# Optimization experiments

Measured on AMD Instinct MI355X. Metric: run time of the kernel, lower is better.

## Reference

```python
import jax, jax.numpy as jnp
import numpy as np

B, SQ, SK, HID, H, D = 2, 2048, 2048, 1024, 16, 64
LN_EPS = 1e-12


def _sinusoid(seq_len):
    # [1,1,S,D]: first half sin, second half cos (RoFormer convention)
    pos = np.arange(seq_len, dtype=np.float32)[:, None]
    inv_freq = 1.0 / (10000.0 ** (np.arange(0, D, 2, dtype=np.float32) / D))
    ang = pos * inv_freq  # [S, D/2]
    return jnp.asarray(np.concatenate([np.sin(ang), np.cos(ang)], axis=-1)[None, None], dtype=jnp.float32)


def setup_inputs() -> dict:
    key = jax.random.key(0)
    ks = jax.random.split(key, 12)
    w = lambda k, shape: jax.random.normal(k, shape, dtype=jnp.float32) * 0.02
    return {
        "hidden_states": jax.random.normal(ks[0], (B, SQ, HID), dtype=jnp.float32),
        "encoder_hidden_states": jax.random.normal(ks[1], (B, SK, HID), dtype=jnp.float32),
        "encoder_attention_mask": jnp.zeros((B, 1, 1, SK), dtype=jnp.float32),  # additive mask
        "sinusoidal_pos": _sinusoid(SQ),
        "c_sinusoidal_pos": _sinusoid(SK),
        "Wq": w(ks[2], (HID, HID)), "bq": jnp.zeros((HID,), jnp.float32),
        "Wk": w(ks[3], (HID, HID)), "bk": jnp.zeros((HID,), jnp.float32),
        "Wv": w(ks[4], (HID, HID)), "bv": jnp.zeros((HID,), jnp.float32),
        "Wd": w(ks[5], (HID, HID)), "bd": jnp.zeros((HID,), jnp.float32),
        "ln_gamma": jnp.ones((HID,), jnp.float32),
        "ln_beta": jnp.zeros((HID,), jnp.float32),
    }


def apply_rope(sinusoidal_pos, layer):
    # sinusoidal_pos: [1,1,S,D] = sin||cos halves; layer: [B,H,S,D]
    sin, cos = jnp.split(sinusoidal_pos, 2, axis=-1)
    sin_pos = jnp.stack([sin, sin], axis=-1).reshape(sinusoidal_pos.shape)
    cos_pos = jnp.stack([cos, cos], axis=-1).reshape(sinusoidal_pos.shape)
    rot = jnp.stack([-layer[..., 1::2], layer[..., ::2]], axis=-1).reshape(layer.shape)
    return layer * cos_pos + rot * sin_pos


def _heads(x):
    b, s, _ = x.shape
    return x.reshape(b, s, H, D).transpose(0, 2, 1, 3)  # [B,H,S,D]


def reference(hidden_states, encoder_hidden_states, encoder_attention_mask,
              sinusoidal_pos, c_sinusoidal_pos,
              Wq, bq, Wk, bk, Wv, bv, Wd, bd, ln_gamma, ln_beta):
    q = _heads(hidden_states @ Wq.T + bq)
    k = _heads(encoder_hidden_states @ Wk.T + bk)
    v = _heads(encoder_hidden_states @ Wv.T + bv)
    q = apply_rope(sinusoidal_pos, q)
    k = apply_rope(c_sinusoidal_pos, k)

    scores = jnp.einsum("bhqd,bhkd->bhqk", q, k) / jnp.sqrt(jnp.float32(D))
    scores = scores + encoder_attention_mask  # broadcast [B,1,1,SK]
    probs = jax.nn.softmax(scores, axis=-1)
    ctx = jnp.einsum("bhqk,bhkd->bhqd", probs, v)
    ctx = ctx.transpose(0, 2, 1, 3).reshape(hidden_states.shape[0], -1, HID)

    proj = ctx @ Wd.T + bd
    x = hidden_states + proj
    mu = jnp.mean(x, axis=-1, keepdims=True)
    var = jnp.mean(jnp.square(x - mu), axis=-1, keepdims=True)
    return (x - mu) / jnp.sqrt(var + LN_EPS) * ln_gamma + ln_beta
```

## Files before the change

### kernel.cpp

```cpp
#include <hip/hip_runtime.h>

typedef __attribute__((ext_vector_type(8))) short short8;
typedef __attribute__((ext_vector_type(4))) float f32x4;
typedef __attribute__((ext_vector_type(16))) float f32x16;

#define LOG2E 1.4426950408889634f
#define QSCALE 0.18033688011112042f

#define ASM_VMCNT2() asm volatile("s_waitcnt vmcnt(2)" ::: "memory")
#define ASM_VMCNT1() asm volatile("s_waitcnt vmcnt(1)" ::: "memory")
#define ASM_VMCNT0() asm volatile("s_waitcnt vmcnt(0)" ::: "memory")
#define ASM_LGKM0()  asm volatile("s_waitcnt lgkmcnt(0)" ::: "memory")

static __device__ __forceinline__ unsigned short f2bf(float f){
  unsigned u = __builtin_bit_cast(unsigned, f);
  u += 0x7FFFu + ((u>>16)&1u);
  return (unsigned short)(u>>16);
}
static __device__ __forceinline__ float bf2f(unsigned short u){
  return __builtin_bit_cast(float, ((unsigned)u)<<16);
}

static __device__ __forceinline__ void async16(const void* g, const void* l){
  __builtin_amdgcn_global_load_lds(
      (const __attribute__((address_space(1))) unsigned*)(unsigned long long)g,
      (__attribute__((address_space(3))) unsigned*)(unsigned)(unsigned long long)l,
      16, 0, 0);
}

__global__ __launch_bounds__(256) void prep_kernel(
    const float* __restrict__ hidden, unsigned short* __restrict__ hb,
    const float* __restrict__ encoder, unsigned short* __restrict__ eb,
    const float* __restrict__ Wq, unsigned short* __restrict__ wqb,
    const float* __restrict__ Wk, unsigned short* __restrict__ wkb,
    const float* __restrict__ Wv, unsigned short* __restrict__ wvb,
    const float* __restrict__ Wd, unsigned short* __restrict__ wdb,
    const float* __restrict__ mask, float* __restrict__ maskE)
{
  int blk = blockIdx.x;
  if (blk < 6144){
    const float* src; unsigned short* dst; int i;
    if (blk < 4096){
      int t = blk*256 + threadIdx.x;
      src = (t >> 19) ? encoder : hidden;
      dst = (t >> 19) ? eb : hb;
      i = (t & 524287)*8;
    } else {
      int t = (blk-4096)*256 + threadIdx.x;
      int z = t >> 17;
      src = (z==0)?Wq:(z==1)?Wk:(z==2)?Wv:Wd;
      dst = (z==0)?wqb:(z==1)?wkb:(z==2)?wvb:wdb;
      i = (t & 131071)*8;
    }
    const float4* s4 = (const float4*)(src + i);
    float4 a = s4[0], b = s4[1];
    union { unsigned short u[8]; short8 v; } o;
    o.u[0]=f2bf(a.x); o.u[1]=f2bf(a.y); o.u[2]=f2bf(a.z); o.u[3]=f2bf(a.w);
    o.u[4]=f2bf(b.x); o.u[5]=f2bf(b.y); o.u[6]=f2bf(b.z); o.u[7]=f2bf(b.w);
    *(short8*)(dst + i) = o.v;
  } else {
    int i = (blk-6144)*256 + threadIdx.x;
    float4 v = ((const float4*)mask)[i];
    v.x*=LOG2E; v.y*=LOG2E; v.z*=LOG2E; v.w*=LOG2E;
    ((float4*)maskE)[i] = v;
  }
}

__global__ __launch_bounds__(512) void gemm_qkv(
    const unsigned short* __restrict__ hb, const unsigned short* __restrict__ eb,
    const unsigned short* __restrict__ wqb, const unsigned short* __restrict__ wkb,
    const unsigned short* __restrict__ wvb,
    const float* __restrict__ bq, const float* __restrict__ bk, const float* __restrict__ bv,
    const float* __restrict__ sp, const float* __restrict__ csp,
    unsigned short* __restrict__ Qb, unsigned short* __restrict__ Kb, unsigned short* __restrict__ Vt)
{
  const int flat = blockIdx.x;
  const int work = (flat&7)*96 + (flat>>3);
  const int bn  = work & 7;
  const int zbm = work >> 3;
  const int z  = zbm >> 5;
  const int bm = zbm & 31;

  const unsigned short* A = (z==0) ? hb : eb;
  const unsigned short* W = (z==0) ? wqb : (z==1 ? wkb : wvb);
  const float* bias = (z==0) ? bq : (z==1 ? bk : bv);
  const float* rope = (z==0) ? sp : (z==1 ? csp : nullptr);

  __shared__ unsigned short As[3][128*32];
  __shared__ unsigned short Bs[3][128*32];

  const int tid = threadIdx.x;
  const int w = tid>>6, l = tid&63;
  const int wr = w>>1, wc = w&1;
  const int srow = tid>>2, scol = (tid&3)*8;

  const f32x4 zero = {0.f,0.f,0.f,0.f};
  f32x4 acc[2][4];
  #pragma unroll
  for (int mi=0;mi<2;mi++)
    #pragma unroll
    for (int ni=0;ni<4;ni++) acc[mi][ni] = zero;

  auto stage = [&](int buf, int kt){
    async16(A + (size_t)(bm*128 + srow)*1024 + kt*32 + scol, As[buf] + tid*8);
    async16(W + (size_t)(bn*128 + srow)*1024 + kt*32 + scol, Bs[buf] + tid*8);
  };

  stage(0, 0);

  int cur = 0;
  for (int kt=0; kt<32; ++kt){
    int nxt = (cur==2) ? 0 : cur+1;
    if (kt < 31){ stage(nxt, kt+1); ASM_VMCNT2(); }
    else        { ASM_VMCNT0(); }
    __builtin_amdgcn_s_barrier();
    __builtin_amdgcn_sched_barrier(0);

    short8 af[2], bf[4];
    #pragma unroll
    for (int mi=0;mi<2;mi++)
      af[mi] = *(const short8*)(As[cur] + (wr*32 + mi*16 + (l&15))*32 + (l>>4)*8);
    #pragma unroll
    for (int ni=0;ni<4;ni++)
      bf[ni] = *(const short8*)(Bs[cur] + (wc*64 + ni*16 + (l&15))*32 + (l>>4)*8);
    #pragma unroll
    for (int mi=0;mi<2;mi++)
      #pragma unroll
      for (int ni=0;ni<4;ni++)
        acc[mi][ni] = __builtin_amdgcn_mfma_f32_16x16x32_bf16(af[mi], bf[ni], acc[mi][ni], 0,0,0);

    cur = nxt;
  }

  if (z == 2){
    #pragma unroll
    for (int mi=0;mi<2;mi++){
      #pragma unroll
      for (int ni=0;ni<4;ni++){
        int mr0 = bm*128 + wr*32 + mi*16 + (l>>4)*4;
        int nc  = bn*128 + wc*64 + ni*16 + (l&15);
        int b0 = mr0>>11, s0 = mr0&2047;
        int h = nc>>6, d = nc&63;
        float bia = bias[nc];
        union { unsigned short u[4]; unsigned long long ull; } pk;
        #pragma unroll
        for (int r=0;r<4;r++) pk.u[r] = f2bf(acc[mi][ni][r] + bia);
        *(unsigned long long*)(Vt + ((size_t)(b0*16 + h)*64 + d)*2048 + s0) = pk.ull;
      }
    }
  } else {
    #pragma unroll
    for (int mi=0;mi<2;mi++){
      #pragma unroll
      for (int ni=0;ni<4;ni++){
        #pragma unroll
        for (int r=0;r<4;r++){
          int mr = bm*128 + wr*32 + mi*16 + (l>>4)*4 + r;
          int nc = bn*128 + wc*64 + ni*16 + (l&15);
          float v = acc[mi][ni][r] + bias[nc];
          int b = mr>>11, s = mr&2047;
          int h = nc>>6,  d = nc&63;
          float p = __shfl_xor(v, 1);
          float sv = rope[s*64 + (d>>1)];
          float cv = rope[s*64 + 32 + (d>>1)];
          float ov = (d&1) ? (v*cv + p*sv) : (v*cv - p*sv);
          if (z == 0) ov *= QSCALE;
          unsigned short* out = (z==0) ? Qb : Kb;
          out[((size_t)(b*16 + h)*2048 + s)*64 + d] = f2bf(ov);
        }
      }
    }
  }
}

__global__ __launch_bounds__(512) void flash_attn(
    const unsigned short* __restrict__ Qb, const unsigned short* __restrict__ Kb,
    const unsigned short* __restrict__ Vt, const float* __restrict__ maskE,
    unsigned short* __restrict__ ctx)
{
  __shared__ unsigned short Kls[2][2][4096];
  __shared__ unsigned short Vls[2][2][4096];
  __shared__ float maskLS[2048];

  const int tid = threadIdx.x;
  const int w = tid>>6, l = tid&63;
  const int qc = l&31, hi = l>>5;
  const int wq = w&3, half = w>>2;

  const int flat = blockIdx.x;
  const int o = (flat&7)*64 + (flat>>3);
  const int qt = o&15, bh = o>>4;
  const int b = bh>>4, h = bh&15;

  {
    ((float4*)maskLS)[tid] = ((const float4*)(maskE + b*2048))[tid];
  }

  const int qrow = qt*128 + wq*32 + qc;
  const unsigned short* qptr = Qb + ((size_t)bh*2048 + qrow)*64;
  short8 qf[4];
  #pragma unroll
  for (int ks=0;ks<4;ks++) qf[ks] = *(const short8*)(qptr + ks*16 + hi*8);

  float m_r = 0.f, l_r = 0.f;
  f32x16 oacc[2];
  #pragma unroll
  for (int t3=0;t3<2;t3++)
    #pragma unroll
    for (int i=0;i<16;i++) oacc[t3][i] = 0.f;

  const int srow = l>>3;
  const int scol = ((l&7) ^ srow)*8;
  const unsigned short* kSrc0; const unsigned short* kSrc1;
  const unsigned short* vSrc0; const unsigned short* vSrc1;
  {
    int c0 = wq*2, c1 = wq*2+1;
    kSrc0 = Kb + ((size_t)bh*2048 + half*1024 + c0*8 + srow)*64 + scol;
    kSrc1 = Kb + ((size_t)bh*2048 + half*1024 + c1*8 + srow)*64 + scol;
    vSrc0 = Vt + ((size_t)bh*64 + c0*8 + srow)*2048 + half*1024 + scol;
    vSrc1 = Vt + ((size_t)bh*64 + c1*8 + srow)*2048 + half*1024 + scol;
  }
  const int ld0 = (wq*2)*512 + l*8, ld1 = (wq*2+1)*512 + l*8;

  auto stage = [&](int buf){
    async16(kSrc0, &Kls[half][buf][ld0]);
    async16(kSrc1, &Kls[half][buf][ld1]);
    async16(vSrc0, &Vls[half][buf][ld0]);
    async16(vSrc1, &Vls[half][buf][ld1]);
    kSrc0 += 4096; kSrc1 += 4096;
    vSrc0 += 64;   vSrc1 += 64;
  };

  stage(0);
  __syncthreads();
  int cur = 0;

  const int rg0 = (qc&7);

  for (int ktl=0; ktl<16; ++ktl){
    if (ktl < 15) stage(cur^1);

    f32x16 sacc[2];
    #pragma unroll
    for (int t2=0;t2<2;t2++){
      #pragma unroll
      for (int rg=0;rg<4;rg++){
        const float4 mv = *(const float4*)&maskLS[half*1024 + ktl*64 + t2*32 + rg*8 + hi*4];
        sacc[t2][rg*4+0] = mv.x;
        sacc[t2][rg*4+1] = mv.y;
        sacc[t2][rg*4+2] = mv.z;
        sacc[t2][rg*4+3] = mv.w;
      }
    }

    __builtin_amdgcn_s_setprio(1);
    #pragma unroll
    for (int ks=0; ks<4; ++ks){
      const short8 kf0 = *(const short8*)(&Kls[half][cur][ qc*64      + (((ks*2+hi)^rg0)*8) ]);
      const short8 kf1 = *(const short8*)(&Kls[half][cur][ (32+qc)*64 + (((ks*2+hi)^rg0)*8) ]);
      sacc[0] = __builtin_amdgcn_mfma_f32_32x32x16_bf16(kf0, qf[ks], sacc[0], 0,0,0);
      sacc[1] = __builtin_amdgcn_mfma_f32_32x32x16_bf16(kf1, qf[ks], sacc[1], 0,0,0);
    }
    __builtin_amdgcn_s_setprio(0);

    float rs = 0.f;
    #pragma unroll
    for (int t2=0;t2<2;t2++)
      #pragma unroll
      for (int i=0;i<16;i++){
        float e = __builtin_amdgcn_exp2f(sacc[t2][i] - m_r);
        sacc[t2][i] = e;
        rs += e;
      }
    { float a = rs, c2 = rs;
      asm("v_permlane32_swap_b32 %0, %1" : "+v"(a), "+v"(c2));
      rs = a + c2; }

    if (__builtin_expect(!__all(rs <= 16777216.0f), 0)){
      float cm = 1.0f;
      #pragma unroll
      for (int t2=0;t2<2;t2++)
        #pragma unroll
        for (int i=0;i<16;i++) cm = fmaxf(cm, sacc[t2][i]);
      { float a = cm, c2 = cm;
        asm("v_permlane32_swap_b32 %0, %1" : "+v"(a), "+v"(c2));
        cm = fmaxf(a, c2); }
      float rin = 1.0f/cm;
      #pragma unroll
      for (int t2=0;t2<2;t2++)
        #pragma unroll
        for (int i=0;i<16;i++) sacc[t2][i] *= rin;
      #pragma unroll
      for (int t3=0;t3<2;t3++)
        #pragma unroll
        for (int i=0;i<16;i++) oacc[t3][i] *= rin;
      l_r *= rin;
      rs  *= rin;
      m_r += log2f(cm);
    }
    l_r += rs;

    short8 pB[4];
    #pragma unroll
    for (int t2=0;t2<2;t2++){
      #pragma unroll
      for (int hf=0; hf<2; ++hf){
        unsigned x0,x1,x2,x3;
        asm("v_cvt_pk_bf16_f32 %0, %1, %2" : "=v"(x0) : "v"(sacc[t2][hf*8+0]), "v"(sacc[t2][hf*8+1]));
        asm("v_cvt_pk_bf16_f32 %0, %1, %2" : "=v"(x1) : "v"(sacc[t2][hf*8+2]), "v"(sacc[t2][hf*8+3]));
        asm("v_cvt_pk_bf16_f32 %0, %1, %2" : "=v"(x2) : "v"(sacc[t2][hf*8+4]), "v"(sacc[t2][hf*8+5]));
        asm("v_cvt_pk_bf16_f32 %0, %1, %2" : "=v"(x3) : "v"(sacc[t2][hf*8+6]), "v"(sacc[t2][hf*8+7]));
        asm("v_permlane32_swap_b32 %0, %1" : "+v"(x2), "+v"(x0));
        asm("v_permlane32_swap_b32 %0, %1" : "+v"(x3), "+v"(x1));
        union { unsigned u[4]; short8 v; } pb;
        pb.u[0]=x0; pb.u[1]=x1; pb.u[2]=x2; pb.u[3]=x3;
        pB[t2*2+hf] = pb.v;
      }
    }

    __builtin_amdgcn_s_setprio(1);
    #pragma unroll
    for (int t3=0;t3<2;t3++){
      #pragma unroll
      for (int si=0; si<4; ++si){
        const short8 vf = *(const short8*)(&Vls[half][cur][ (t3*32+qc)*64 + (((si*2+hi)^rg0)*8) ]);
        oacc[t3] = __builtin_amdgcn_mfma_f32_32x32x16_bf16(vf, pB[si], oacc[t3], 0,0,0);
      }
    }
    __builtin_amdgcn_s_setprio(0);

    __syncthreads();
    cur ^= 1;
  }

  float* Ox  = (float*)&Kls[0][0][0];
  float* MLf = (float*)&Vls[0][0][0];

  if (half == 1){
    #pragma unroll
    for (int t3=0;t3<2;t3++){
      #pragma unroll
      for (int rg=0;rg<4;rg++){
        int dbase = t3*32 + rg*8 + hi*4;
        f32x4 o4 = { oacc[t3][rg*4+0], oacc[t3][rg*4+1], oacc[t3][rg*4+2], oacc[t3][rg*4+3] };
        *(f32x4*)&Ox[wq*2048 + qc*64 + (dbase ^ (rg0*8))] = o4;
      }
    }
    if (hi == 0){
      MLf[wq*64 + qc]      = m_r;
      MLf[wq*64 + 32 + qc] = l_r;
    }
  }
  __syncthreads();

  if (half == 0){
    float m1 = MLf[wq*64 + qc];
    float l1 = MLf[wq*64 + 32 + qc];
    float mstar = fmaxf(m_r, m1);
    float s0 = __builtin_amdgcn_exp2f(m_r - mstar);
    float s1 = __builtin_amdgcn_exp2f(m1 - mstar);
    float inv = 1.0f / (l_r*s0 + l1*s1);
    float a0 = s0*inv, a1 = s1*inv;

    int qglob = qt*128 + wq*32 + qc;
    unsigned short* cp = ctx + ((size_t)b*2048 + qglob)*1024 + h*64;
    #pragma unroll
    for (int t3=0;t3<2;t3++){
      #pragma unroll
      for (int rg=0;rg<4;rg++){
        int dbase = t3*32 + rg*8 + hi*4;
        f32x4 o1 = *(const f32x4*)&Ox[wq*2048 + qc*64 + (dbase ^ (rg0*8))];
        union { unsigned short u[4]; unsigned long long ull; } pk4;
        #pragma unroll
        for (int i=0;i<4;i++) pk4.u[i] = f2bf(oacc[t3][rg*4+i]*a0 + o1[i]*a1);
        *(unsigned long long*)(cp + dbase) = pk4.ull;
      }
    }
  }
}

__global__ __launch_bounds__(512) void gemm_proj(
    const unsigned short* __restrict__ ctxb, const unsigned short* __restrict__ wdb,
    const float* __restrict__ bd, const unsigned short* __restrict__ hb,
    unsigned short* __restrict__ X)
{
  const int flat = blockIdx.x;
  const int work = (flat&7)*64 + (flat>>3);
  const int bn = work & 7;
  const int bm = work >> 3;

  __shared__ unsigned short As[3][64*32];
  __shared__ unsigned short Bs[3][128*32];
  const int tid = threadIdx.x;
  const int w = tid>>6, l = tid&63;
  const int wr = w>>2, wc = w&3;

  const f32x4 zero = {0.f,0.f,0.f,0.f};
  f32x4 acc[2][2];
  #pragma unroll
  for (int mi=0;mi<2;mi++)
    #pragma unroll
    for (int ni=0;ni<2;ni++) acc[mi][ni] = zero;

  auto stage = [&](int buf, int kt){
    if (tid < 256)
      async16(ctxb + (size_t)(bm*64 + (tid>>2))*1024 + kt*32 + (tid&3)*8, As[buf] + tid*8);
    async16(wdb + (size_t)(bn*128 + (tid>>2))*1024 + kt*32 + (tid&3)*8, Bs[buf] + tid*8);
  };

  stage(0, 0);

  int cur = 0;
  for (int kt=0; kt<32; ++kt){
    int nxt = (cur==2) ? 0 : cur+1;
    if (kt < 31){
      stage(nxt, kt+1);
      if (w < 4) ASM_VMCNT2(); else ASM_VMCNT1();
    } else {
      ASM_VMCNT0();
    }
    __builtin_amdgcn_s_barrier();
    __builtin_amdgcn_sched_barrier(0);

    short8 af[2], bf[2];
    #pragma unroll
    for (int mi=0;mi<2;mi++)
      af[mi] = *(const short8*)(As[cur] + (wr*32 + mi*16 + (l&15))*32 + (l>>4)*8);
    #pragma unroll
    for (int ni=0;ni<2;ni++)
      bf[ni] = *(const short8*)(Bs[cur] + (wc*32 + ni*16 + (l&15))*32 + (l>>4)*8);
    #pragma unroll
    for (int mi=0;mi<2;mi++)
      #pragma unroll
      for (int ni=0;ni<2;ni++)
        acc[mi][ni] = __builtin_amdgcn_mfma_f32_16x16x32_bf16(af[mi], bf[ni], acc[mi][ni], 0,0,0);

    cur = nxt;
  }

  #pragma unroll
  for (int mi=0;mi<2;mi++){
    #pragma unroll
    for (int ni=0;ni<2;ni++){
      #pragma unroll
      for (int r=0;r<4;r++){
        int mr = bm*64 + wr*32 + mi*16 + (l>>4)*4 + r;
        int nc = bn*128 + wc*32 + ni*16 + (l&15);
        float v = acc[mi][ni][r] + bd[nc] + bf2f(hb[(size_t)mr*1024 + nc]);
        X[(size_t)mr*1024 + nc] = f2bf(v);
      }
    }
  }
}

__global__ __launch_bounds__(256) void ln_kernel(
    const unsigned short* __restrict__ X, const float* __restrict__ gamma,
    const float* __restrict__ beta, float* __restrict__ out)
{
  const int row = blockIdx.x;
  const int tid = threadIdx.x;
  uint2 raw = ((const uint2*)(X + (size_t)row*1024))[tid];
  float v0 = __builtin_bit_cast(float, (raw.x & 0xFFFFu) << 16);
  float v1 = __builtin_bit_cast(float, raw.x & 0xFFFF0000u);
  float v2 = __builtin_bit_cast(float, (raw.y & 0xFFFFu) << 16);
  float v3 = __builtin_bit_cast(float, raw.y & 0xFFFF0000u);
  float s  = v0+v1+v2+v3;
  float ss = v0*v0 + v1*v1 + v2*v2 + v3*v3;
  #pragma unroll
  for (int off=1; off<64; off<<=1){
    s  += __shfl_xor(s, off);
    ss += __shfl_xor(ss, off);
  }
  __shared__ float red[8];
  const int w = tid>>6, l = tid&63;
  if (l == 0){ red[w] = s; red[4+w] = ss; }
  __syncthreads();
  s  = red[0]+red[1]+red[2]+red[3];
  ss = red[4]+red[5]+red[6]+red[7];
  float mu  = s*(1.f/1024.f);
  float var = ss*(1.f/1024.f) - mu*mu;
  float inv = rsqrtf(var + 1e-12f);
  const float4 g  = ((const float4*)gamma)[tid];
  const float4 bt = ((const float4*)beta)[tid];
  float4 oo;
  oo.x = (v0-mu)*inv*g.x + bt.x;
  oo.y = (v1-mu)*inv*g.y + bt.y;
  oo.z = (v2-mu)*inv*g.z + bt.z;
  oo.w = (v3-mu)*inv*g.w + bt.w;
  ((float4*)(out + (size_t)row*1024))[tid] = oo;
}

extern "C" void kernel_launch(void* const* d_in, const int* in_sizes, int n_in,
                              void* d_out, int out_size, void* d_ws, size_t ws_size,
                              hipStream_t stream) {
  const float* hidden  = (const float*)d_in[0];
  const float* encoder = (const float*)d_in[1];
  const float* mask    = (const float*)d_in[2];
  const float* sp      = (const float*)d_in[3];
  const float* csp     = (const float*)d_in[4];
  const float* Wq = (const float*)d_in[5];  const float* bq = (const float*)d_in[6];
  const float* Wk = (const float*)d_in[7];  const float* bk = (const float*)d_in[8];
  const float* Wv = (const float*)d_in[9];  const float* bv = (const float*)d_in[10];
  const float* Wd = (const float*)d_in[11]; const float* bd = (const float*)d_in[12];
  const float* gamma = (const float*)d_in[13];
  const float* beta  = (const float*)d_in[14];

  char* ws = (char*)d_ws;
  const size_t MB_ = 1ull<<20;
  unsigned short* hb  = (unsigned short*)(ws + 0);
  unsigned short* eb  = (unsigned short*)(ws + 8*MB_);
  unsigned short* wqb = (unsigned short*)(ws + 16*MB_);
  unsigned short* wkb = (unsigned short*)(ws + 18*MB_);
  unsigned short* wvb = (unsigned short*)(ws + 20*MB_);
  unsigned short* wdb = (unsigned short*)(ws + 22*MB_);
  unsigned short* Qb  = (unsigned short*)(ws + 24*MB_);
  unsigned short* Kb  = (unsigned short*)(ws + 32*MB_);
  unsigned short* Vt  = (unsigned short*)(ws + 40*MB_);
  unsigned short* ctxb = eb;
  unsigned short* X = Qb;
  float* maskE = (float*)(ws + 48*MB_);

  prep_kernel<<<6148,256,0,stream>>>(hidden, hb, encoder, eb,
                                     Wq, wqb, Wk, wkb, Wv, wvb, Wd, wdb,
                                     mask, maskE);

  gemm_qkv<<<768,512,0,stream>>>(hb, eb, wqb, wkb, wvb,
                                 bq, bk, bv, sp, csp, Qb, Kb, Vt);
  flash_attn<<<512,512,0,stream>>>(Qb, Kb, Vt, maskE, ctxb);
  gemm_proj<<<512,512,0,stream>>>(ctxb, wdb, bd, hb, X);
  ln_kernel<<<4096,256,0,stream>>>(X, gamma, beta, (float*)d_out);
}
```

Before: 120.9 us.

## Single-buffer V, store mask as bf16, and replace block syncs with vmcnt waits

The attention kernel keeps K double-buffered but gives V a single LDS buffer. The additive mask is stored in LDS as bf16 instead of fp32. Per-tile __syncthreads is replaced by an s_barrier plus per-wave s_waitcnt vmcnt waits, with the V load issued at the top of each iteration and waited on just before the PV MFMAs. This shrinks the LDS footprint, allowing more resident blocks per CU, and lets V loads overlap QK compute. The costs are V no longer being prefetched a full tile ahead, reduced mask precision, and a possible cross-wave visibility race, since each wave waits only on its own async loads.

```diff
diff --git a/kernel.cpp b/kernel.cpp
--- a/kernel.cpp
+++ b/kernel.cpp
@@ -7,6 +7,7 @@
 #define LOG2E 1.4426950408889634f
 #define QSCALE 0.18033688011112042f
 
+#define ASM_VMCNT4() asm volatile("s_waitcnt vmcnt(4)" ::: "memory")
 #define ASM_VMCNT2() asm volatile("s_waitcnt vmcnt(2)" ::: "memory")
 #define ASM_VMCNT1() asm volatile("s_waitcnt vmcnt(1)" ::: "memory")
 #define ASM_VMCNT0() asm volatile("s_waitcnt vmcnt(0)" ::: "memory")
@@ -179,8 +180,8 @@
     unsigned short* __restrict__ ctx)
 {
   __shared__ unsigned short Kls[2][2][4096];
-  __shared__ unsigned short Vls[2][2][4096];
-  __shared__ float maskLS[2048];
+  __shared__ unsigned short Vls[2][4096];
+  __shared__ unsigned short maskB[2048];
 
   const int tid = threadIdx.x;
   const int w = tid>>6, l = tid&63;
@@ -193,7 +194,11 @@
   const int b = bh>>4, h = bh&15;
 
   {
-    ((float4*)maskLS)[tid] = ((const float4*)(maskE + b*2048))[tid];
+    float4 mv = ((const float4*)(maskE + b*2048))[tid];
+    unsigned x0, x1;
+    asm("v_cvt_pk_bf16_f32 %0, %1, %2" : "=v"(x0) : "v"(mv.x), "v"(mv.y));
+    asm("v_cvt_pk_bf16_f32 %0, %1, %2" : "=v"(x1) : "v"(mv.z), "v"(mv.w));
+    *(uint2*)&maskB[tid*4] = make_uint2(x0, x1);
   }
 
   const int qrow = qt*128 + wq*32 + qc;
@@ -222,34 +227,39 @@
   }
   const int ld0 = (wq*2)*512 + l*8, ld1 = (wq*2+1)*512 + l*8;
 
-  auto stage = [&](int buf){
-    async16(kSrc0, &Kls[half][buf][ld0]);
-    async16(kSrc1, &Kls[half][buf][ld1]);
-    async16(vSrc0, &Vls[half][buf][ld0]);
-    async16(vSrc1, &Vls[half][buf][ld1]);
-    kSrc0 += 4096; kSrc1 += 4096;
-    vSrc0 += 64;   vSrc1 += 64;
-  };
-
-  stage(0);
-  __syncthreads();
+  async16(kSrc0, &Kls[half][0][ld0]);
+  async16(kSrc1, &Kls[half][0][ld1]);
+  kSrc0 += 4096; kSrc1 += 4096;
+  ASM_LGKM0();
+
   int cur = 0;
-
   const int rg0 = (qc&7);
 
   for (int ktl=0; ktl<16; ++ktl){
-    if (ktl < 15) stage(cur^1);
+    __builtin_amdgcn_s_barrier();
+    async16(vSrc0, &Vls[half][ld0]);
+    async16(vSrc1, &Vls[half][ld1]);
+    vSrc0 += 64; vSrc1 += 64;
+    if (ktl < 15){
+      async16(kSrc0, &Kls[half][cur^1][ld0]);
+      async16(kSrc1, &Kls[half][cur^1][ld1]);
+      kSrc0 += 4096; kSrc1 += 4096;
+      ASM_VMCNT4();
+    } else {
+      ASM_VMCNT2();
+    }
+    __builtin_amdgcn_sched_barrier(0);
 
     f32x16 sacc[2];
     #pragma unroll
     for (int t2=0;t2<2;t2++){
       #pragma unroll
       for (int rg=0;rg<4;rg++){
-        const float4 mv = *(const float4*)&maskLS[half*1024 + ktl*64 + t2*32 + rg*8 + hi*4];
-        sacc[t2][rg*4+0] = mv.x;
-        sacc[t2][rg*4+1] = mv.y;
-        sacc[t2][rg*4+2] = mv.z;
-        sacc[t2][rg*4+3] = mv.w;
+        uint2 raw = *(const uint2*)&maskB[half*1024 + ktl*64 + t2*32 + rg*8 + hi*4];
+        sacc[t2][rg*4+0] = __builtin_bit_cast(float, raw.x << 16);
+        sacc[t2][rg*4+1] = __builtin_bit_cast(float, raw.x & 0xFFFF0000u);
+        sacc[t2][rg*4+2] = __builtin_bit_cast(float, raw.y << 16);
+        sacc[t2][rg*4+3] = __builtin_bit_cast(float, raw.y & 0xFFFF0000u);
       }
     }
 
@@ -318,23 +328,27 @@
       }
     }
 
+    if (ktl < 15) ASM_VMCNT2();
+    else         ASM_VMCNT0();
+    __builtin_amdgcn_sched_barrier(0);
+
     __builtin_amdgcn_s_setprio(1);
     #pragma unroll
     for (int t3=0;t3<2;t3++){
       #pragma unroll
       for (int si=0; si<4; ++si){
-        const short8 vf = *(const short8*)(&Vls[half][cur][ (t3*32+qc)*64 + (((si*2+hi)^rg0)*8) ]);
+        const short8 vf = *(const short8*)(&Vls[half][ (t3*32+qc)*64 + (((si*2+hi)^rg0)*8) ]);
         oacc[t3] = __builtin_amdgcn_mfma_f32_32x32x16_bf16(vf, pB[si], oacc[t3], 0,0,0);
       }
     }
     __builtin_amdgcn_s_setprio(0);
 
-    __syncthreads();
     cur ^= 1;
   }
+  __syncthreads();
 
   float* Ox  = (float*)&Kls[0][0][0];
-  float* MLf = (float*)&Vls[0][0][0];
+  float* MLf = (float*)&Vls[0][0];
 
   if (half == 1){
     #pragma unroll
```

Result: slower. 126.7 us (+4.9%).
